# Kernel optimization log

Hardware: AMD Instinct MI355X
Metric: run time of the kernel (lower is better)

Reference implementation:

```python
import jax, jax.numpy as jnp
import numpy as np


def _aggregate(x, w, k, pad):
    """Involution-style per-pixel local conv.
    x: [N, C, H, W]; w: [N, heads, wc, k*k, H, W] (stride=1, dilation=1, zero pad).
    Returns [N, heads, C, H, W].
    """
    N, C, H, W = x.shape
    heads, wc = w.shape[1], w.shape[2]
    G = C // wc  # channel groups sharing the same per-pixel weights (c % wc)
    xp = jnp.pad(x, ((0, 0), (0, 0), (pad, pad), (pad, pad)))
    # unfold: [N, C, k*k, H, W] via k*k static shifted slices (no dynamic indexing)
    patches = jnp.stack(
        [xp[:, :, i:i + H, j:j + W] for i in range(k) for j in range(k)], axis=2
    )
    p = patches.reshape(N, G, wc, k * k, H, W)
    # out[n, e, g, v, h, w] = sum_k w[n, e, v, k, h, w] * p[n, g, v, k, h, w]
    out = jnp.einsum('nevkhw,ngvkhw->negvhw', w, p)
    return out.reshape(N, heads, C, H, W)


def reference(x, weight1, weight2):
    out1 = _aggregate(x, weight1, 3, 1)  # 3x3 branch, pad=1
    out2 = _aggregate(x, weight2, 5, 2)  # 5x5 branch, pad=2
    # output layout [N, 2, heads, C, H, W] matching the CUDA index arithmetic
    return jnp.stack([out1, out2], axis=1)


def setup_inputs() -> dict:
    key = jax.random.key(0)
    k1, k2, k3 = jax.random.split(key, 3)
    N, C, H, W = 4, 256, 56, 56
    heads, wc = 1, 32
    x = jax.random.normal(k1, (N, C, H, W), dtype=jnp.float32)
    weight1 = jax.random.normal(k2, (N, heads, wc, 9, H, W), dtype=jnp.float32)
    weight2 = jax.random.normal(k3, (N, heads, wc, 25, H, W), dtype=jnp.float32)
    return {"x": x, "weight1": weight1, "weight2": weight2}
```

## Files before the change

kernel.cpp:

```cpp
#include <hip/hip_runtime.h>


#define N_  4
#define C_  256
#define H_  56
#define W_  56
#define HW_ 3136
#define WC_ 32

#define TILE    14
#define LROWS   18
#define LSTRIDE 68

__global__ __launch_bounds__(256) void lconv_kernel(
    const float* __restrict__ x,
    const float* __restrict__ w1,
    const float* __restrict__ w2,
    float* __restrict__ out)
{
    __shared__ float lds[4 * LROWS * LSTRIDE];

    const int b     = blockIdx.x;
    const int tile  = b & 3;
    const int vlow  = (b >> 2) & 1;
    const int gsel  = (b >> 3) & 1;
    const int vhigh = (b >> 4) & 15;
    const int n     = b >> 8;
    const int v     = (vhigh << 1) | vlow;
    const int r0    = tile * TILE;
    const int nv    = n * WC_ + v;
    const int tid   = threadIdx.x;

    for (int idx = tid; idx < 4 * LROWS * 14; idx += 256) {
        const int c4 = idx % 14;
        const int t2 = idx / 14;
        const int lr = t2 % LROWS;
        const int pl = t2 / LROWS;
        const int gr = r0 - 2 + lr;
        float4 val = make_float4(0.f, 0.f, 0.f, 0.f);
        if (gr >= 0 && gr < H_) {
            const int ch = gsel * 128 + pl * 32 + v;
            val = *(const float4*)(x + (size_t)(n * C_ + ch) * HW_ + gr * W_ + c4 * 4);
        }
        float* lp = &lds[(pl * LROWS + lr) * LSTRIDE + 4 * c4 + 2];
        *(float2*)(lp)     = make_float2(val.x, val.y);
        *(float2*)(lp + 2) = make_float2(val.z, val.w);
    }
    for (int idx = tid; idx < 4 * LROWS * 4; idx += 256) {
        const int k  = idx & 3;
        const int t2 = idx >> 2;
        const int lr = t2 % LROWS;
        const int pl = t2 / LROWS;
        const int slot = (k < 2) ? k : (56 + k);
        lds[(pl * LROWS + lr) * LSTRIDE + slot] = 0.f;
    }
    __syncthreads();

    if (tid >= TILE * 14) return;

    const int row = tid / 14;
    const int s   = tid - row * 14;
    const int wb  = 4 * s;
    const int h   = r0 + row;
    const int hw  = h * W_ + wb;

    const float* w1t = w1 + (size_t)nv * 9  * HW_ + hw;
    const float* w2t = w2 + (size_t)nv * 25 * HW_ + hw;
    const int c0 = gsel * 128 + v;

    float a2[4][4];
    #pragma unroll
    for (int g = 0; g < 4; ++g)
        #pragma unroll
        for (int p = 0; p < 4; ++p) a2[g][p] = 0.f;

    float4 w2cur[5], w2nxt[5];
    #pragma unroll
    for (int dj = 0; dj < 5; ++dj)
        w2cur[dj] = *(const float4*)(w2t + (size_t)dj * HW_);

    #pragma unroll 1
    for (int di = 0; di < 5; ++di) {
        if (di < 4) {
            #pragma unroll
            for (int dj = 0; dj < 5; ++dj)
                w2nxt[dj] = *(const float4*)(w2t + (size_t)((di + 1) * 5 + dj) * HW_);
        }
        #pragma unroll
        for (int g = 0; g < 4; ++g) {
            const float* lp = &lds[(g * LROWS + row + di) * LSTRIDE + wb];
            const float4 xa  = *(const float4*)(lp);
            const float4 xb4 = *(const float4*)(lp + 4);
            const float xw[8] = {xa.x, xa.y, xa.z, xa.w, xb4.x, xb4.y, xb4.z, xb4.w};
            #pragma unroll
            for (int dj = 0; dj < 5; ++dj) {
                const float* wr = (const float*)&w2cur[dj];
                #pragma unroll
                for (int p = 0; p < 4; ++p)
                    a2[g][p] += wr[p] * xw[p + dj];
            }
        }
        if (di < 4) {
            #pragma unroll
            for (int dj = 0; dj < 5; ++dj) w2cur[dj] = w2nxt[dj];
        }
    }

    float* o2 = out + ((size_t)(n * 2 + 1) * C_ + c0) * HW_ + hw;
    #pragma unroll
    for (int g = 0; g < 4; ++g)
        *(float4*)(o2 + (size_t)g * WC_ * HW_) =
            make_float4(a2[g][0], a2[g][1], a2[g][2], a2[g][3]);

    float a1[4][4];
    #pragma unroll
    for (int g = 0; g < 4; ++g)
        #pragma unroll
        for (int p = 0; p < 4; ++p) a1[g][p] = 0.f;

    float4 w1cur[3], w1nxt[3];
    #pragma unroll
    for (int dj = 0; dj < 3; ++dj)
        w1cur[dj] = *(const float4*)(w1t + (size_t)dj * HW_);

    #pragma unroll 1
    for (int di = 0; di < 3; ++di) {
        if (di < 2) {
            #pragma unroll
            for (int dj = 0; dj < 3; ++dj)
                w1nxt[dj] = *(const float4*)(w1t + (size_t)((di + 1) * 3 + dj) * HW_);
        }
        #pragma unroll
        for (int g = 0; g < 4; ++g) {
            const float* lp = &lds[(g * LROWS + row + 1 + di) * LSTRIDE + wb];
            const float4 xa  = *(const float4*)(lp);
            const float4 xb4 = *(const float4*)(lp + 4);
            const float xw[8] = {xa.x, xa.y, xa.z, xa.w, xb4.x, xb4.y, xb4.z, xb4.w};
            #pragma unroll
            for (int dj = 0; dj < 3; ++dj) {
                const float* wr = (const float*)&w1cur[dj];
                #pragma unroll
                for (int p = 0; p < 4; ++p)
                    a1[g][p] += wr[p] * xw[p + dj + 1];
            }
        }
        if (di < 2) {
            #pragma unroll
            for (int dj = 0; dj < 3; ++dj) w1cur[dj] = w1nxt[dj];
        }
    }

    float* o1 = out + ((size_t)(n * 2 + 0) * C_ + c0) * HW_ + hw;
    #pragma unroll
    for (int g = 0; g < 4; ++g)
        *(float4*)(o1 + (size_t)g * WC_ * HW_) =
            make_float4(a1[g][0], a1[g][1], a1[g][2], a1[g][3]);
}

extern "C" void kernel_launch(void* const* d_in, const int* in_sizes, int n_in,
                              void* d_out, int out_size, void* d_ws, size_t ws_size,
                              hipStream_t stream) {
    const float* x  = (const float*)d_in[0];
    const float* w1 = (const float*)d_in[1];
    const float* w2 = (const float*)d_in[2];
    float* out = (float*)d_out;

    dim3 grid(1024), block(256);
    hipLaunchKernelGGL(lconv_kernel, grid, block, 0, stream, x, w1, w2, out);
}
```

Before: 113.2 us.

## Retile blocks to 7 rows with all 8 channel groups and reorder block index

```diff
diff --git a/kernel.cpp b/kernel.cpp
--- a/kernel.cpp
+++ b/kernel.cpp
@@ -8,8 +8,9 @@
 #define HW_ 3136
 #define WC_ 32
 
-#define TILE    14
-#define LROWS   18
+#define TILE    7
+#define LROWS   11
+#define NPL     8
 #define LSTRIDE 68
 
 __global__ __launch_bounds__(256) void lconv_kernel(
@@ -18,20 +19,17 @@
     const float* __restrict__ w2,
     float* __restrict__ out)
 {
-    __shared__ float lds[4 * LROWS * LSTRIDE];
+    __shared__ float lds[NPL * LROWS * LSTRIDE];
 
-    const int b     = blockIdx.x;
-    const int tile  = b & 3;
-    const int vlow  = (b >> 2) & 1;
-    const int gsel  = (b >> 3) & 1;
-    const int vhigh = (b >> 4) & 15;
-    const int n     = b >> 8;
-    const int v     = (vhigh << 1) | vlow;
-    const int r0    = tile * TILE;
-    const int nv    = n * WC_ + v;
-    const int tid   = threadIdx.x;
+    const int b    = blockIdx.x;
+    const int v    = b & 31;
+    const int n    = (b >> 5) & 3;
+    const int tile = b >> 7;
+    const int r0   = tile * TILE;
+    const int nv   = n * WC_ + v;
+    const int tid  = threadIdx.x;
 
-    for (int idx = tid; idx < 4 * LROWS * 14; idx += 256) {
+    for (int idx = tid; idx < NPL * LROWS * 14; idx += 256) {
         const int c4 = idx % 14;
         const int t2 = idx / 14;
         const int lr = t2 % LROWS;
@@ -39,14 +37,14 @@
         const int gr = r0 - 2 + lr;
         float4 val = make_float4(0.f, 0.f, 0.f, 0.f);
         if (gr >= 0 && gr < H_) {
-            const int ch = gsel * 128 + pl * 32 + v;
+            const int ch = pl * WC_ + v;
             val = *(const float4*)(x + (size_t)(n * C_ + ch) * HW_ + gr * W_ + c4 * 4);
         }
         float* lp = &lds[(pl * LROWS + lr) * LSTRIDE + 4 * c4 + 2];
         *(float2*)(lp)     = make_float2(val.x, val.y);
         *(float2*)(lp + 2) = make_float2(val.z, val.w);
     }
-    for (int idx = tid; idx < 4 * LROWS * 4; idx += 256) {
+    for (int idx = tid; idx < NPL * LROWS * 4; idx += 256) {
         const int k  = idx & 3;
         const int t2 = idx >> 2;
         const int lr = t2 % LROWS;
@@ -56,17 +54,20 @@
     }
     __syncthreads();
 
-    if (tid >= TILE * 14) return;
+    if (tid >= 2 * TILE * 14) return;
 
-    const int row = tid / 14;
-    const int s   = tid - row * 14;
-    const int wb  = 4 * s;
-    const int h   = r0 + row;
-    const int hw  = h * W_ + wb;
+    const int ghalf = (tid >= TILE * 14) ? 1 : 0;
+    const int t     = tid - ghalf * TILE * 14;
+    const int row   = t / 14;
+    const int s     = t - row * 14;
+    const int wb    = 4 * s;
+    const int gb    = ghalf * 4;
+    const int h     = r0 + row;
+    const int hw    = h * W_ + wb;
 
     const float* w1t = w1 + (size_t)nv * 9  * HW_ + hw;
     const float* w2t = w2 + (size_t)nv * 25 * HW_ + hw;
-    const int c0 = gsel * 128 + v;
+    const int c0 = gb * WC_ + v;
 
     float a2[4][4];
     #pragma unroll
@@ -88,7 +89,7 @@
         }
         #pragma unroll
         for (int g = 0; g < 4; ++g) {
-            const float* lp = &lds[(g * LROWS + row + di) * LSTRIDE + wb];
+            const float* lp = &lds[((gb + g) * LROWS + row + di) * LSTRIDE + wb];
             const float4 xa  = *(const float4*)(lp);
             const float4 xb4 = *(const float4*)(lp + 4);
             const float xw[8] = {xa.x, xa.y, xa.z, xa.w, xb4.x, xb4.y, xb4.z, xb4.w};
@@ -132,7 +133,7 @@
         }
         #pragma unroll
         for (int g = 0; g < 4; ++g) {
-            const float* lp = &lds[(g * LROWS + row + 1 + di) * LSTRIDE + wb];
+            const float* lp = &lds[((gb + g) * LROWS + row + 1 + di) * LSTRIDE + wb];
             const float4 xa  = *(const float4*)(lp);
             const float4 xb4 = *(const float4*)(lp + 4);
             const float xw[8] = {xa.x, xa.y, xa.z, xa.w, xb4.x, xb4.y, xb4.z, xb4.w};
```

After: 115.2 us. Within noise of the previous version (+1.8%).

## Drop LDS tiling; map one thread per channel-row 8-pixel segment reading global directly

Applied to the files above, without the earlier changes.

```diff
diff --git a/kernel.cpp b/kernel.cpp
--- a/kernel.cpp
+++ b/kernel.cpp
@@ -8,153 +8,142 @@
 #define HW_ 3136
 #define WC_ 32
 
-#define TILE    14
-#define LROWS   18
-#define LSTRIDE 68
-
 __global__ __launch_bounds__(256) void lconv_kernel(
     const float* __restrict__ x,
     const float* __restrict__ w1,
     const float* __restrict__ w2,
     float* __restrict__ out)
 {
-    __shared__ float lds[4 * LROWS * LSTRIDE];
+    const int gid  = blockIdx.x * 256 + threadIdx.x;
+    const int wseg = gid % 7;
+    int t = gid / 7;
+    const int h = t % H_;
+    t /= H_;
+    const int c = t & (C_ - 1);
+    const int n = t >> 8;
+    const int v = c & (WC_ - 1);
+    const int wb = wseg * 8;
+    const int hw = h * W_ + wb;
 
-    const int b     = blockIdx.x;
-    const int tile  = b & 3;
-    const int vlow  = (b >> 2) & 1;
-    const int gsel  = (b >> 3) & 1;
-    const int vhigh = (b >> 4) & 15;
-    const int n     = b >> 8;
-    const int v     = (vhigh << 1) | vlow;
-    const int r0    = tile * TILE;
-    const int nv    = n * WC_ + v;
-    const int tid   = threadIdx.x;
+    const float* xpl = x + (size_t)(n * C_ + c) * HW_;
+    const float* w2t = w2 + (size_t)(n * WC_ + v) * 25 * HW_ + hw;
+    const float* w1t = w1 + (size_t)(n * WC_ + v) * 9  * HW_ + hw;
 
-    for (int idx = tid; idx < 4 * LROWS * 14; idx += 256) {
-        const int c4 = idx % 14;
-        const int t2 = idx / 14;
-        const int lr = t2 % LROWS;
-        const int pl = t2 / LROWS;
-        const int gr = r0 - 2 + lr;
-        float4 val = make_float4(0.f, 0.f, 0.f, 0.f);
-        if (gr >= 0 && gr < H_) {
-            const int ch = gsel * 128 + pl * 32 + v;
-            val = *(const float4*)(x + (size_t)(n * C_ + ch) * HW_ + gr * W_ + c4 * 4);
-        }
-        float* lp = &lds[(pl * LROWS + lr) * LSTRIDE + 4 * c4 + 2];
-        *(float2*)(lp)     = make_float2(val.x, val.y);
-        *(float2*)(lp + 2) = make_float2(val.z, val.w);
+    float a2[8];
+    #pragma unroll
+    for (int p = 0; p < 8; ++p) a2[p] = 0.f;
+
+    float4 wcur[10], wnxt[10];
+    #pragma unroll
+    for (int dj = 0; dj < 5; ++dj) {
+        wcur[2*dj]   = *(const float4*)(w2t + (size_t)dj * HW_);
+        wcur[2*dj+1] = *(const float4*)(w2t + (size_t)dj * HW_ + 4);
     }
-    for (int idx = tid; idx < 4 * LROWS * 4; idx += 256) {
-        const int k  = idx & 3;
-        const int t2 = idx >> 2;
-        const int lr = t2 % LROWS;
-        const int pl = t2 / LROWS;
-        const int slot = (k < 2) ? k : (56 + k);
-        lds[(pl * LROWS + lr) * LSTRIDE + slot] = 0.f;
-    }
-    __syncthreads();
-
-    if (tid >= TILE * 14) return;
-
-    const int row = tid / 14;
-    const int s   = tid - row * 14;
-    const int wb  = 4 * s;
-    const int h   = r0 + row;
-    const int hw  = h * W_ + wb;
-
-    const float* w1t = w1 + (size_t)nv * 9  * HW_ + hw;
-    const float* w2t = w2 + (size_t)nv * 25 * HW_ + hw;
-    const int c0 = gsel * 128 + v;
-
-    float a2[4][4];
-    #pragma unroll
-    for (int g = 0; g < 4; ++g)
-        #pragma unroll
-        for (int p = 0; p < 4; ++p) a2[g][p] = 0.f;
-
-    float4 w2cur[5], w2nxt[5];
-    #pragma unroll
-    for (int dj = 0; dj < 5; ++dj)
-        w2cur[dj] = *(const float4*)(w2t + (size_t)dj * HW_);
 
     #pragma unroll 1
     for (int di = 0; di < 5; ++di) {
         if (di < 4) {
             #pragma unroll
-            for (int dj = 0; dj < 5; ++dj)
-                w2nxt[dj] = *(const float4*)(w2t + (size_t)((di + 1) * 5 + dj) * HW_);
+            for (int dj = 0; dj < 5; ++dj) {
+                wnxt[2*dj]   = *(const float4*)(w2t + (size_t)((di+1)*5 + dj) * HW_);
+                wnxt[2*dj+1] = *(const float4*)(w2t + (size_t)((di+1)*5 + dj) * HW_ + 4);
+            }
+        }
+        float xw[12];
+        const int xr = h - 2 + di;
+        if (xr >= 0 && xr < H_) {
+            const float* xp = xpl + xr * W_ + wb;
+            const float4 xb4 = *(const float4*)(xp);
+            const float4 xc4 = *(const float4*)(xp + 4);
+            float2 xa2 = make_float2(0.f, 0.f);
+            float2 xd2 = make_float2(0.f, 0.f);
+            if (wseg > 0) xa2 = *(const float2*)(xp - 2);
+            if (wseg < 6) xd2 = *(const float2*)(xp + 8);
+            xw[0]  = xa2.x; xw[1]  = xa2.y;
+            xw[2]  = xb4.x; xw[3]  = xb4.y; xw[4] = xb4.z; xw[5] = xb4.w;
+            xw[6]  = xc4.x; xw[7]  = xc4.y; xw[8] = xc4.z; xw[9] = xc4.w;
+            xw[10] = xd2.x; xw[11] = xd2.y;
+        } else {
+            #pragma unroll
+            for (int q = 0; q < 12; ++q) xw[q] = 0.f;
         }
         #pragma unroll
-        for (int g = 0; g < 4; ++g) {
-            const float* lp = &lds[(g * LROWS + row + di) * LSTRIDE + wb];
-            const float4 xa  = *(const float4*)(lp);
-            const float4 xb4 = *(const float4*)(lp + 4);
-            const float xw[8] = {xa.x, xa.y, xa.z, xa.w, xb4.x, xb4.y, xb4.z, xb4.w};
+        for (int dj = 0; dj < 5; ++dj) {
+            const float* wlo = (const float*)&wcur[2*dj];
+            const float* whi = (const float*)&wcur[2*dj+1];
             #pragma unroll
-            for (int dj = 0; dj < 5; ++dj) {
-                const float* wr = (const float*)&w2cur[dj];
-                #pragma unroll
-                for (int p = 0; p < 4; ++p)
-                    a2[g][p] += wr[p] * xw[p + dj];
+            for (int p = 0; p < 4; ++p) {
+                a2[p]     += wlo[p] * xw[p + dj];
+                a2[p + 4] += whi[p] * xw[p + 4 + dj];
             }
         }
         if (di < 4) {
             #pragma unroll
-            for (int dj = 0; dj < 5; ++dj) w2cur[dj] = w2nxt[dj];
+            for (int q = 0; q < 10; ++q) wcur[q] = wnxt[q];
         }
     }
 
-    float* o2 = out + ((size_t)(n * 2 + 1) * C_ + c0) * HW_ + hw;
+    float* o2 = out + ((size_t)(n * 2 + 1) * C_ + c) * HW_ + hw;
+    *(float4*)(o2)     = make_float4(a2[0], a2[1], a2[2], a2[3]);
+    *(float4*)(o2 + 4) = make_float4(a2[4], a2[5], a2[6], a2[7]);
+
+    float a1[8];
     #pragma unroll
-    for (int g = 0; g < 4; ++g)
-        *(float4*)(o2 + (size_t)g * WC_ * HW_) =
-            make_float4(a2[g][0], a2[g][1], a2[g][2], a2[g][3]);
+    for (int p = 0; p < 8; ++p) a1[p] = 0.f;
 
-    float a1[4][4];
+    float4 vcur[6], vnxt[6];
     #pragma unroll
-    for (int g = 0; g < 4; ++g)
-        #pragma unroll
-        for (int p = 0; p < 4; ++p) a1[g][p] = 0.f;
-
-    float4 w1cur[3], w1nxt[3];
-    #pragma unroll
-    for (int dj = 0; dj < 3; ++dj)
-        w1cur[dj] = *(const float4*)(w1t + (size_t)dj * HW_);
+    for (int dj = 0; dj < 3; ++dj) {
+        vcur[2*dj]   = *(const float4*)(w1t + (size_t)dj * HW_);
+        vcur[2*dj+1] = *(const float4*)(w1t + (size_t)dj * HW_ + 4);
+    }
 
     #pragma unroll 1
     for (int di = 0; di < 3; ++di) {
         if (di < 2) {
             #pragma unroll
-            for (int dj = 0; dj < 3; ++dj)
-                w1nxt[dj] = *(const float4*)(w1t + (size_t)((di + 1) * 3 + dj) * HW_);
+            for (int dj = 0; dj < 3; ++dj) {
+                vnxt[2*dj]   = *(const float4*)(w1t + (size_t)((di+1)*3 + dj) * HW_);
+                vnxt[2*dj+1] = *(const float4*)(w1t + (size_t)((di+1)*3 + dj) * HW_ + 4);
+            }
+        }
+        float xw[12];
+        const int xr = h - 1 + di;
+        if (xr >= 0 && xr < H_) {
+            const float* xp = xpl + xr * W_ + wb;
+            const float4 xb4 = *(const float4*)(xp);
+            const float4 xc4 = *(const float4*)(xp + 4);
+            float2 xa2 = make_float2(0.f, 0.f);
+            float2 xd2 = make_float2(0.f, 0.f);
+            if (wseg > 0) xa2 = *(const float2*)(xp - 2);
+            if (wseg < 6) xd2 = *(const float2*)(xp + 8);
+            xw[0]  = xa2.x; xw[1]  = xa2.y;
+            xw[2]  = xb4.x; xw[3]  = xb4.y; xw[4] = xb4.z; xw[5] = xb4.w;
+            xw[6]  = xc4.x; xw[7]  = xc4.y; xw[8] = xc4.z; xw[9] = xc4.w;
+            xw[10] = xd2.x; xw[11] = xd2.y;
+        } else {
+            #pragma unroll
+            for (int q = 0; q < 12; ++q) xw[q] = 0.f;
         }
         #pragma unroll
-        for (int g = 0; g < 4; ++g) {
-            const float* lp = &lds[(g * LROWS + row + 1 + di) * LSTRIDE + wb];
-            const float4 xa  = *(const float4*)(lp);
-            const float4 xb4 = *(const float4*)(lp + 4);
-            const float xw[8] = {xa.x, xa.y, xa.z, xa.w, xb4.x, xb4.y, xb4.z, xb4.w};
+        for (int dj = 0; dj < 3; ++dj) {
+            const float* wlo = (const float*)&vcur[2*dj];
+            const float* whi = (const float*)&vcur[2*dj+1];
             #pragma unroll
-            for (int dj = 0; dj < 3; ++dj) {
-                const float* wr = (const float*)&w1cur[dj];
-                #pragma unroll
-                for (int p = 0; p < 4; ++p)
-                    a1[g][p] += wr[p] * xw[p + dj + 1];
+            for (int p = 0; p < 4; ++p) {
+                a1[p]     += wlo[p] * xw[p + dj + 1];
+                a1[p + 4] += whi[p] * xw[p + dj + 5];
             }
         }
         if (di < 2) {
             #pragma unroll
-            for (int dj = 0; dj < 3; ++dj) w1cur[dj] = w1nxt[dj];
+            for (int q = 0; q < 6; ++q) vcur[q] = vnxt[q];
         }
     }
 
-    float* o1 = out + ((size_t)(n * 2 + 0) * C_ + c0) * HW_ + hw;
-    #pragma unroll
-    for (int g = 0; g < 4; ++g)
-        *(float4*)(o1 + (size_t)g * WC_ * HW_) =
-            make_float4(a1[g][0], a1[g][1], a1[g][2], a1[g][3]);
+    float* o1 = out + ((size_t)(n * 2 + 0) * C_ + c) * HW_ + hw;
+    *(float4*)(o1)     = make_float4(a1[0], a1[1], a1[2], a1[3]);
+    *(float4*)(o1 + 4) = make_float4(a1[4], a1[5], a1[6], a1[7]);
 }
 
 extern "C" void kernel_launch(void* const* d_in, const int* in_sizes, int n_in,
@@ -165,6 +154,6 @@
     const float* w2 = (const float*)d_in[2];
     float* out = (float*)d_out;
 
-    dim3 grid(1024), block(256);
+    dim3 grid(1568), block(256);
     hipLaunchKernelGGL(lconv_kernel, grid, block, 0, stream, x, w1, w2, out);
 }
```

Result: slower. 154.7 us (+36.8%).
